# Kernel tuning notes

Measured on AMD Instinct MI355X. Metric: run time of the kernel, lower is better.

## Reference

```python
import jax, jax.numpy as jnp
import numpy as np

N_NODES = 3_000_000  # divisible by 3 (x.view(-1, 3))
N_EDGES = 48_000_000  # avg degree 16


def setup_inputs() -> dict:
    key = jax.random.key(0)
    ks = jax.random.split(key, 8)
    x = jax.random.normal(ks[0], (N_NODES, 1), dtype=jnp.float32)
    edge_index = jax.random.randint(ks[1], (2, N_EDGES), 0, N_NODES, dtype=jnp.int64)
    # SAGEConv(1, 1, bias=False): lin_l applied to aggregated neighbors, lin_r to root
    W_l = jax.random.normal(ks[2], (1, 1), dtype=jnp.float32)
    W_r = jax.random.normal(ks[3], (1, 1), dtype=jnp.float32)
    # nn.Sequential(Linear(1,2), ReLU, Linear(2,1)) with default biases
    W1 = jax.random.normal(ks[4], (2, 1), dtype=jnp.float32)
    b1 = jax.random.normal(ks[5], (2,), dtype=jnp.float32)
    W2 = jax.random.normal(ks[6], (1, 2), dtype=jnp.float32)
    b2 = jax.random.normal(ks[7], (1,), dtype=jnp.float32)
    return {"x": x, "edge_index": edge_index, "W_l": W_l, "W_r": W_r,
            "W1": W1, "b1": b1, "W2": W2, "b2": b2}


def reference(x, edge_index, W_l, W_r, W1, b1, W2, b2):
    src, dst = edge_index[0], edge_index[1]
    # sum-aggregate messages x_j from source nodes onto target nodes
    agg = jax.ops.segment_sum(x[src], dst, num_segments=N_NODES)  # [N, 1]
    # SAGEConv: lin_l(agg) + lin_r(x)
    h = agg @ W_l.T + x @ W_r.T  # [N, 1]
    # x.view(-1, 3)[:, 0] -> take every 3rd node's feature
    h0 = h.reshape(-1, 3)[:, 0:1]  # [N/3, 1]
    # MLP: Linear(1,2) -> ReLU -> Linear(2,1)
    out = jax.nn.relu(h0 @ W1.T + b1) @ W2.T + b2  # [N/3, 1]
    return out.reshape(-1)
```

## Files before the change

### kernel.cpp

```cpp
#include <hip/hip_runtime.h>


static constexpr int kNodes = 3000000;
static constexpr int kEdges = 48000000;
static constexpr int kOut   = 1000000;

__global__ __launch_bounds__(256) void edge_scatter(
    const int* __restrict__ ei,
    const float* __restrict__ x,
    float* __restrict__ agg)
{
    const int tid = blockIdx.x * blockDim.x + threadIdx.x;
    const int e = tid * 4;
    if (e >= kEdges) return;

    const int4 s4 = *reinterpret_cast<const int4*>(ei + e);
    const int4 d4 = *reinterpret_cast<const int4*>(ei + kEdges + e);

    const int ss[4] = {s4.x, s4.y, s4.z, s4.w};
    const int dd[4] = {d4.x, d4.y, d4.z, d4.w};

#pragma unroll
    for (int k = 0; k < 4; ++k) {
        const unsigned d = (unsigned)dd[k];
        const unsigned q = d / 3u;
        if (q * 3u == d) {
            atomicAdd(agg + q, x[ss[k]]);
        }
    }
}

__global__ __launch_bounds__(256) void finalize(
    const float* __restrict__ agg,
    const float* __restrict__ x,
    const float* __restrict__ Wl,
    const float* __restrict__ Wr,
    const float* __restrict__ W1,
    const float* __restrict__ b1,
    const float* __restrict__ W2,
    const float* __restrict__ b2,
    float* __restrict__ out)
{
    const int j = blockIdx.x * blockDim.x + threadIdx.x;
    if (j >= kOut) return;

    const float wl  = Wl[0];
    const float wr  = Wr[0];
    const float w10 = W1[0];
    const float w11 = W1[1];
    const float bb0 = b1[0];
    const float bb1 = b1[1];
    const float w20 = W2[0];
    const float w21 = W2[1];
    const float bb2 = b2[0];

    const float h = agg[j] * wl + x[3 * j] * wr;
    const float t0 = fmaxf(h * w10 + bb0, 0.0f);
    const float t1 = fmaxf(h * w11 + bb1, 0.0f);
    out[j] = t0 * w20 + t1 * w21 + bb2;
}

extern "C" void kernel_launch(void* const* d_in, const int* in_sizes, int n_in,
                              void* d_out, int out_size, void* d_ws, size_t ws_size,
                              hipStream_t stream)
{
    const float* x  = (const float*)d_in[0];
    const int*   ei = (const int*)d_in[1];
    const float* Wl = (const float*)d_in[2];
    const float* Wr = (const float*)d_in[3];
    const float* W1 = (const float*)d_in[4];
    const float* b1 = (const float*)d_in[5];
    const float* W2 = (const float*)d_in[6];
    const float* b2 = (const float*)d_in[7];
    float* out = (float*)d_out;

    float* agg = (float*)d_ws;

    hipMemsetAsync(agg, 0, kOut * sizeof(float), stream);

    const int nThreads = kEdges / 4;
    edge_scatter<<<nThreads / 256, 256, 0, stream>>>(ei, x, agg);

    finalize<<<(kOut + 255) / 256, 256, 0, stream>>>(agg, x, Wl, Wr, W1, b1, W2, b2, out);
}
```

Before: 1.180 ms.

## Privatize scatter accumulators per XCC and stream edge indices with nontemporal loads

Gives each XCC (read from a hardware register) its own copy of the aggregation buffer. Scatter atomics become workgroup-scope, so they can resolve in that XCC's L2 instead of being coherent across the whole device. The finalize kernel sums the 8 copies before applying the MLP. Edge-index loads become nontemporal so they do not pollute the cache. In exchange the memset grows to eight buffers and finalize reads eight times as much data, and the change relies on kernel-boundary cache writeback for correctness across XCCs. It falls back to the single-buffer path if the workspace is too small.

New measurement: 1.206 ms. +2.2%, slower.

```diff
diff --git a/kernel.cpp b/kernel.cpp
--- a/kernel.cpp
+++ b/kernel.cpp
@@ -1,11 +1,44 @@
 #include <hip/hip_runtime.h>
 
 
-static constexpr int kNodes = 3000000;
 static constexpr int kEdges = 48000000;
 static constexpr int kOut   = 1000000;
 
-__global__ __launch_bounds__(256) void edge_scatter(
+typedef int v4i __attribute__((ext_vector_type(4)));
+
+__device__ __forceinline__ unsigned xcc_id() {
+    return (unsigned)__builtin_amdgcn_s_getreg((3 << 11) | 20) & 7u;
+}
+
+__global__ __launch_bounds__(256) void edge_scatter_priv(
+    const int* __restrict__ ei,
+    const float* __restrict__ x,
+    float* __restrict__ copies)
+{
+    const int tid = blockIdx.x * blockDim.x + threadIdx.x;
+    const int e = tid * 4;
+    if (e >= kEdges) return;
+
+    float* myagg = copies + (size_t)xcc_id() * kOut;
+
+    const v4i s4 = __builtin_nontemporal_load(reinterpret_cast<const v4i*>(ei + e));
+    const v4i d4 = __builtin_nontemporal_load(reinterpret_cast<const v4i*>(ei + kEdges + e));
+
+    const int ss[4] = {s4.x, s4.y, s4.z, s4.w};
+    const int dd[4] = {d4.x, d4.y, d4.z, d4.w};
+
+#pragma unroll
+    for (int k = 0; k < 4; ++k) {
+        const unsigned d = (unsigned)dd[k];
+        const unsigned q = d / 3u;
+        if (q * 3u == d) {
+            __hip_atomic_fetch_add(myagg + q, x[ss[k]],
+                                   __ATOMIC_RELAXED, __HIP_MEMORY_SCOPE_WORKGROUP);
+        }
+    }
+}
+
+__global__ __launch_bounds__(256) void edge_scatter_dev(
     const int* __restrict__ ei,
     const float* __restrict__ x,
     float* __restrict__ agg)
@@ -14,8 +47,8 @@
     const int e = tid * 4;
     if (e >= kEdges) return;
 
-    const int4 s4 = *reinterpret_cast<const int4*>(ei + e);
-    const int4 d4 = *reinterpret_cast<const int4*>(ei + kEdges + e);
+    const v4i s4 = __builtin_nontemporal_load(reinterpret_cast<const v4i*>(ei + e));
+    const v4i d4 = __builtin_nontemporal_load(reinterpret_cast<const v4i*>(ei + kEdges + e));
 
     const int ss[4] = {s4.x, s4.y, s4.z, s4.w};
     const int dd[4] = {d4.x, d4.y, d4.z, d4.w};
@@ -31,7 +64,7 @@
 }
 
 __global__ __launch_bounds__(256) void finalize(
-    const float* __restrict__ agg,
+    const float* __restrict__ copies, int ncopies,
     const float* __restrict__ x,
     const float* __restrict__ Wl,
     const float* __restrict__ Wr,
@@ -44,20 +77,14 @@
     const int j = blockIdx.x * blockDim.x + threadIdx.x;
     if (j >= kOut) return;
 
-    const float wl  = Wl[0];
-    const float wr  = Wr[0];
-    const float w10 = W1[0];
-    const float w11 = W1[1];
-    const float bb0 = b1[0];
-    const float bb1 = b1[1];
-    const float w20 = W2[0];
-    const float w21 = W2[1];
-    const float bb2 = b2[0];
+    float a = 0.0f;
+    for (int c = 0; c < ncopies; ++c)
+        a += copies[(size_t)c * kOut + j];
 
-    const float h = agg[j] * wl + x[3 * j] * wr;
-    const float t0 = fmaxf(h * w10 + bb0, 0.0f);
-    const float t1 = fmaxf(h * w11 + bb1, 0.0f);
-    out[j] = t0 * w20 + t1 * w21 + bb2;
+    const float h = a * Wl[0] + x[3 * j] * Wr[0];
+    const float t0 = fmaxf(h * W1[0] + b1[0], 0.0f);
+    const float t1 = fmaxf(h * W1[1] + b1[1], 0.0f);
+    out[j] = t0 * W2[0] + t1 * W2[1] + b2[0];
 }
 
 extern "C" void kernel_launch(void* const* d_in, const int* in_sizes, int n_in,
@@ -74,12 +101,19 @@
     const float* b2 = (const float*)d_in[7];
     float* out = (float*)d_out;
 
-    float* agg = (float*)d_ws;
+    float* copies = (float*)d_ws;
+    const size_t needPriv = 8ull * kOut * sizeof(float);
 
-    hipMemsetAsync(agg, 0, kOut * sizeof(float), stream);
+    const int nScatterBlocks = (kEdges / 4) / 256;
+    const int nFinBlocks = (kOut + 255) / 256;
 
-    const int nThreads = kEdges / 4;
-    edge_scatter<<<nThreads / 256, 256, 0, stream>>>(ei, x, agg);
-
-    finalize<<<(kOut + 255) / 256, 256, 0, stream>>>(agg, x, Wl, Wr, W1, b1, W2, b2, out);
+    if (ws_size >= needPriv) {
+        hipMemsetAsync(copies, 0, needPriv, stream);
+        edge_scatter_priv<<<nScatterBlocks, 256, 0, stream>>>(ei, x, copies);
+        finalize<<<nFinBlocks, 256, 0, stream>>>(copies, 8, x, Wl, Wr, W1, b1, W2, b2, out);
+    } else {
+        hipMemsetAsync(copies, 0, kOut * sizeof(float), stream);
+        edge_scatter_dev<<<nScatterBlocks, 256, 0, stream>>>(ei, x, copies);
+        finalize<<<nFinBlocks, 256, 0, stream>>>(copies, 1, x, Wl, Wr, W1, b1, W2, b2, out);
+    }
 }
```
